# Optimization experiments

Hardware: AMD Instinct MI355X
Metric: run time of the kernel (lower is better)

Reference implementation:

```python
import jax, jax.numpy as jnp
import numpy as np

STRIDE = 4.0      # fpn_strides[0]
POOL = 7          # roi_align_size
SR = 2            # roi_align_sampling_ratio
NUM_CLASSES = 10
B, N = 2, 512
C, H, W = 256, 256, 256
OUT = 1024


def _bilinear(feat_hwc, y, x):
    # feat_hwc: [H, W, C]; y, x: [N, 7, 7, SR, SR] sample coords (feature units)
    Hf, Wf, _ = feat_hwc.shape
    valid = (y > -1.0) & (y < Hf) & (x > -1.0) & (x < Wf)
    y = jnp.clip(y, 0.0, Hf - 1.0)
    x = jnp.clip(x, 0.0, Wf - 1.0)
    y0 = jnp.floor(y)
    x0 = jnp.floor(x)
    y0i = y0.astype(jnp.int32)
    x0i = x0.astype(jnp.int32)
    y1i = jnp.minimum(y0i + 1, Hf - 1)
    x1i = jnp.minimum(x0i + 1, Wf - 1)
    ly = (y - y0)[..., None]
    lx = (x - x0)[..., None]
    hy = 1.0 - ly
    hx = 1.0 - lx
    v = (hy * hx * feat_hwc[y0i, x0i] + hy * lx * feat_hwc[y0i, x1i]
         + ly * hx * feat_hwc[y1i, x0i] + ly * lx * feat_hwc[y1i, x1i])
    return v * valid[..., None]


def _roi_align_rotated(feat_hwc, boxes):
    # boxes: [N, 5] = (cx, cy, w, h, theta) in feature coords -> [N, 7, 7, C]
    cx, cy, w, h, th = (boxes[:, k] for k in range(5))
    bins = jnp.arange(POOL, dtype=feat_hwc.dtype)
    sub = (jnp.arange(SR, dtype=feat_hwc.dtype) + 0.5) / SR
    # local (box-frame) coords of sample points along each axis: [N, 7, SR]
    ys = -h[:, None, None] / 2 + (h / POOL)[:, None, None] * (bins[None, :, None] + sub[None, None, :])
    xs = -w[:, None, None] / 2 + (w / POOL)[:, None, None] * (bins[None, :, None] + sub[None, None, :])
    yy = ys[:, :, None, :, None]  # [N,7,1,SR,1]
    xx = xs[:, None, :, None, :]  # [N,1,7,1,SR]
    cos = jnp.cos(th)[:, None, None, None, None]
    sin = jnp.sin(th)[:, None, None, None, None]
    gx = cx[:, None, None, None, None] + xx * cos - yy * sin
    gy = cy[:, None, None, None, None] + xx * sin + yy * cos
    v = _bilinear(feat_hwc, gy, gx)  # [N,7,7,SR,SR,C]
    return v.mean(axis=(3, 4))       # average-pool the SRxSR samples per bin


def norm_angle(a):
    return (a + jnp.pi / 2) % jnp.pi - jnp.pi / 2


def setup_inputs():
    key = jax.random.key(0)
    ks = jax.random.split(key, 14)
    feat = jax.random.normal(ks[0], (B, C, H, W), jnp.float32)
    cx = jax.random.uniform(ks[1], (B, N), minval=16.0, maxval=H - 16.0)
    cy = jax.random.uniform(ks[2], (B, N), minval=16.0, maxval=W - 16.0)
    bw = jax.random.uniform(ks[3], (B, N), minval=8.0, maxval=64.0)
    bh = jax.random.uniform(ks[4], (B, N), minval=8.0, maxval=64.0)
    th = jax.random.uniform(ks[5], (B, N), minval=-np.pi / 2, maxval=np.pi / 2)
    proposals = jnp.stack([cx, cy, bw, bh, th], axis=-1).astype(jnp.float32)
    d_in = C * POOL * POOL
    s = 0.02
    return {
        'feat': feat,
        'proposals': proposals,
        'W1': jax.random.normal(ks[6], (d_in, OUT), jnp.float32) * s,
        'b1': jnp.zeros((OUT,), jnp.float32),
        'W2': jax.random.normal(ks[7], (OUT, OUT), jnp.float32) * s,
        'b2': jnp.zeros((OUT,), jnp.float32),
        'Wcls': jax.random.normal(ks[8], (OUT, NUM_CLASSES + 1), jnp.float32) * s,
        'bcls': jnp.zeros((NUM_CLASSES + 1,), jnp.float32),
        'Wreg': jax.random.normal(ks[9], (OUT, 5), jnp.float32) * s,
        'breg': jnp.zeros((5,), jnp.float32),
    }


def reference(feat, proposals, W1, b1, W2, b2, Wcls, bcls, Wreg, breg):
    Bn, Nn = proposals.shape[:2]
    feat_hwc = jnp.transpose(feat, (0, 2, 3, 1))  # [B,H,W,C]
    pooled = jax.vmap(_roi_align_rotated)(feat_hwc, proposals)  # [B,N,7,7,C]
    # torch flattens [N, C, 7, 7] -> C*49; match that layout
    x = jnp.transpose(pooled, (0, 1, 4, 2, 3)).reshape(Bn, Nn, -1)
    x = jax.nn.relu(x @ W1 + b1)
    x = jax.nn.relu(x @ W2 + b2)
    cls = x @ Wcls + bcls   # [B,N,11]
    reg = x @ Wreg + breg   # [B,N,5]
    # decode (proposals scaled to image coords by stride; theta unscaled)
    scale = jnp.array([STRIDE, STRIDE, STRIDE, STRIDE, 1.0], feat.dtype)
    p = proposals * scale
    clamp_v = float(abs(np.log(16.0 / 1000.0)))
    bx = p[..., 2] * reg[..., 0] + p[..., 0]
    by = p[..., 3] * reg[..., 1] + p[..., 1]
    bw = p[..., 2] * jnp.exp(jnp.clip(reg[..., 2], -clamp_v, clamp_v))
    bh = p[..., 3] * jnp.exp(jnp.clip(reg[..., 3], -clamp_v, clamp_v))
    ba = norm_angle(p[..., 4] + reg[..., 4])
    boxes = jnp.stack([bx, by, bw, bh, ba], axis=-1)
    return boxes, cls
```

## Files before the change

kernel.cpp:

```cpp
#include <hip/hip_runtime.h>
#include <math.h>
#include <stdint.h>

#define BB 2
#define NN 512
#define CC 256
#define HH 256
#define WW 256
#define DIN 12544
#define OUT1 1024
#define NCLS 11
#define NROI 1024
#define SK1 8
#define SK2 2

typedef short bf16x8 __attribute__((ext_vector_type(8)));
typedef float f32x4 __attribute__((ext_vector_type(4)));

__device__ inline unsigned short f2bf(float f) {
  unsigned int u = __float_as_uint(f);
  u += 0x7FFF + ((u >> 16) & 1);
  return (unsigned short)(u >> 16);
}
__device__ inline float bf2f(unsigned short h) {
  return __uint_as_float(((unsigned int)h) << 16);
}
__device__ inline float4 ld_bf4(const unsigned short* p) {
  ushort4 r = *(const ushort4*)p;
  return make_float4(bf2f(r.x), bf2f(r.y), bf2f(r.z), bf2f(r.w));
}

__device__ inline void gll16(const void* g, void* l) {
  __builtin_amdgcn_global_load_lds(
      reinterpret_cast<const __attribute__((address_space(1))) void*>(
          reinterpret_cast<uintptr_t>(g)),
      reinterpret_cast<__attribute__((address_space(3))) void*>(
          (unsigned int)reinterpret_cast<uintptr_t>(l)),
      16, 0, 0);
}

__global__ __launch_bounds__(256) void transpose_to_hwc_bf16(
    const float* __restrict__ in, unsigned short* __restrict__ out) {
  __shared__ float tile[64][65];
  int b = blockIdx.z;
  int hw0 = blockIdx.x * 64;
  int c0 = blockIdx.y * 64;
  int tid = threadIdx.x;
  int hi = tid >> 4, lo = tid & 15;
#pragma unroll
  for (int pass = 0; pass < 4; ++pass) {
    int cl = hi + pass * 16;
    float4 v = *(const float4*)(in + ((size_t)b * CC + c0 + cl) * (HH * WW) +
                                hw0 + lo * 4);
    tile[lo * 4 + 0][cl] = v.x;
    tile[lo * 4 + 1][cl] = v.y;
    tile[lo * 4 + 2][cl] = v.z;
    tile[lo * 4 + 3][cl] = v.w;
  }
  __syncthreads();
#pragma unroll
  for (int pass = 0; pass < 4; ++pass) {
    int hwl = hi + pass * 16;
    int cc = lo * 4;
    ushort4 o;
    o.x = f2bf(tile[hwl][cc + 0]);
    o.y = f2bf(tile[hwl][cc + 1]);
    o.z = f2bf(tile[hwl][cc + 2]);
    o.w = f2bf(tile[hwl][cc + 3]);
    *(ushort4*)(out + ((size_t)b * (HH * WW) + hw0 + hwl) * CC + c0 + cc) = o;
  }
}

__device__ inline void bilin(float gy, float gx, int& y0, int& x0, int& y1,
                             int& x1, float& w00, float& w01, float& w10,
                             float& w11) {
  float valid = (gy > -1.f && gy < 256.f && gx > -1.f && gx < 256.f) ? 0.25f : 0.f;
  float y = fminf(fmaxf(gy, 0.f), 255.f);
  float x = fminf(fmaxf(gx, 0.f), 255.f);
  float yf = floorf(y), xf = floorf(x);
  y0 = (int)yf; x0 = (int)xf;
  y1 = min(y0 + 1, 255); x1 = min(x0 + 1, 255);
  float ly = y - yf, lx = x - xf, hy = 1.f - ly, hx = 1.f - lx;
  w00 = hy * hx * valid; w01 = hy * lx * valid;
  w10 = ly * hx * valid; w11 = ly * lx * valid;
}

__global__ __launch_bounds__(256) void roi_align_hwc(
    const unsigned short* __restrict__ fhwc, const float* __restrict__ props,
    unsigned short* __restrict__ pooled) {
  int roi = blockIdx.x;
  int b = roi >> 9;
  const float* p = props + (size_t)roi * 5;
  float cx = p[0], cy = p[1], w = p[2], h = p[3], th = p[4];
  float sn = sinf(th), cs = cosf(th);
  int wave = threadIdx.x >> 6, lane = threadIdx.x & 63;
  int c4 = lane * 4;
  const unsigned short* fb = fhwc + (size_t)b * HH * WW * CC;
  unsigned short* outp = pooled + (size_t)roi * DIN;

  for (int bin = wave; bin < 49; bin += 4) {
    int py = bin / 7, px = bin - py * 7;
    float a0 = 0.f, a1 = 0.f, a2 = 0.f, a3 = 0.f;
#pragma unroll
    for (int sy = 0; sy < 2; ++sy) {
#pragma unroll
      for (int sx = 0; sx < 2; ++sx) {
        float ys = -0.5f * h + (h / 7.0f) * ((float)py + ((float)sy + 0.5f) * 0.5f);
        float xs = -0.5f * w + (w / 7.0f) * ((float)px + ((float)sx + 0.5f) * 0.5f);
        float gx = cx + xs * cs - ys * sn;
        float gy = cy + xs * sn + ys * cs;
        int y0, x0, y1, x1; float w00, w01, w10, w11;
        bilin(gy, gx, y0, x0, y1, x1, w00, w01, w10, w11);
        float4 v00 = ld_bf4(fb + ((size_t)(y0 * WW + x0)) * CC + c4);
        float4 v01 = ld_bf4(fb + ((size_t)(y0 * WW + x1)) * CC + c4);
        float4 v10 = ld_bf4(fb + ((size_t)(y1 * WW + x0)) * CC + c4);
        float4 v11 = ld_bf4(fb + ((size_t)(y1 * WW + x1)) * CC + c4);
        a0 += w00 * v00.x + w01 * v01.x + w10 * v10.x + w11 * v11.x;
        a1 += w00 * v00.y + w01 * v01.y + w10 * v10.y + w11 * v11.y;
        a2 += w00 * v00.z + w01 * v01.z + w10 * v10.z + w11 * v11.z;
        a3 += w00 * v00.w + w01 * v01.w + w10 * v10.w + w11 * v11.w;
      }
    }
    ushort4 o;
    o.x = f2bf(a0); o.y = f2bf(a1); o.z = f2bf(a2); o.w = f2bf(a3);
    *(ushort4*)(outp + bin * 256 + c4) = o;
  }
}

__global__ __launch_bounds__(256) void roi_align_nchw(
    const float* __restrict__ feat, const float* __restrict__ props,
    unsigned short* __restrict__ pooled) {
  int roi = blockIdx.x;
  int b = roi >> 9;
  int c = threadIdx.x;
  const float* p = props + (size_t)roi * 5;
  float cx = p[0], cy = p[1], w = p[2], h = p[3], th = p[4];
  float sn = sinf(th), cs = cosf(th);
  const float* fb = feat + ((size_t)b * CC + c) * (HH * WW);
  unsigned short* outp = pooled + (size_t)roi * DIN;
  for (int bin = 0; bin < 49; ++bin) {
    int py = bin / 7, px = bin - py * 7;
    float acc = 0.f;
#pragma unroll
    for (int sy = 0; sy < 2; ++sy) {
#pragma unroll
      for (int sx = 0; sx < 2; ++sx) {
        float ys = -0.5f * h + (h / 7.0f) * ((float)py + ((float)sy + 0.5f) * 0.5f);
        float xs = -0.5f * w + (w / 7.0f) * ((float)px + ((float)sx + 0.5f) * 0.5f);
        float gx = cx + xs * cs - ys * sn;
        float gy = cy + xs * sn + ys * cs;
        int y0, x0, y1, x1; float w00, w01, w10, w11;
        bilin(gy, gx, y0, x0, y1, x1, w00, w01, w10, w11);
        acc += w00 * fb[(size_t)y0 * WW + x0] + w01 * fb[(size_t)y0 * WW + x1] +
               w10 * fb[(size_t)y1 * WW + x0] + w11 * fb[(size_t)y1 * WW + x1];
      }
    }
    outp[bin * 256 + c] = f2bf(acc);
  }
}

template <bool PERM>
__global__ __launch_bounds__(256) void cvt_w(const float* __restrict__ in,
                                             unsigned short* __restrict__ out,
                                             int N, int Kout) {
  __shared__ float tile[64][65];
  int k0 = blockIdx.x * 64, n0 = blockIdx.y * 64;
  int tid = threadIdx.x;
  int hi = tid >> 4, lo = tid & 15;
#pragma unroll
  for (int pass = 0; pass < 4; ++pass) {
    int ki = hi + pass * 16;
    int k = k0 + ki;
    int row = PERM ? ((k & 255) * 49 + (k >> 8)) : k;
    float4 v = *(const float4*)(in + (size_t)row * N + n0 + lo * 4);
    tile[ki][lo * 4 + 0] = v.x;
    tile[ki][lo * 4 + 1] = v.y;
    tile[ki][lo * 4 + 2] = v.z;
    tile[ki][lo * 4 + 3] = v.w;
  }
  __syncthreads();
#pragma unroll
  for (int pass = 0; pass < 4; ++pass) {
    int nl = hi + pass * 16;
    int kq = lo * 4;
    ushort4 o;
    o.x = f2bf(tile[kq + 0][nl]);
    o.y = f2bf(tile[kq + 1][nl]);
    o.z = f2bf(tile[kq + 2][nl]);
    o.w = f2bf(tile[kq + 3][nl]);
    *(ushort4*)(out + (size_t)(n0 + nl) * Kout + k0 + kq) = o;
  }
}

__global__ __launch_bounds__(256) void pack_head_w(
    const float* __restrict__ Wcls, const float* __restrict__ bcls,
    const float* __restrict__ Wreg, const float* __restrict__ breg,
    unsigned short* __restrict__ Wcat, float* __restrict__ bcat) {
  int o = blockIdx.x;
  int t = threadIdx.x;
#pragma unroll
  for (int j = 0; j < 4; ++j) {
    int k = t * 4 + j;
    float v = (o < NCLS) ? Wcls[(size_t)k * NCLS + o]
                         : Wreg[(size_t)k * 5 + (o - NCLS)];
    Wcat[(size_t)o * OUT1 + k] = f2bf(v);
  }
  if (t == 0) bcat[o] = (o < NCLS) ? bcls[o] : breg[o - NCLS];
}

__global__ __launch_bounds__(256) void gemm_mfma_128(
    const unsigned short* __restrict__ A, const unsigned short* __restrict__ Bw,
    unsigned short* __restrict__ part, int K, int Ks) {
  __shared__ short As[128 * 32];
  __shared__ short Bs[128 * 32];
  int tid = threadIdx.x;
  int w = tid >> 6, lane = tid & 63;
  int quad = lane >> 4, l16 = lane & 15;
  int m0 = blockIdx.y * 128, n0 = blockIdx.x * 128;
  int bz = blockIdx.z;
  int wm = w >> 1, wn = w & 1;

  const char* pA = (const char*)A +
      ((size_t)(m0 + 32 * w + (lane >> 2)) * K + (size_t)bz * Ks) * 2 +
      (lane & 3) * 16;
  const char* pB = (const char*)Bw +
      ((size_t)(n0 + 32 * w + (lane >> 2)) * K + (size_t)bz * Ks) * 2 +
      (lane & 3) * 16;
  short* la = &As[w * 1024];
  short* lb = &Bs[w * 1024];
  const size_t rstep = (size_t)K * 2 * 16;

  f32x4 acc[4][4] = {};
  int aoff[4], boff[4];
#pragma unroll
  for (int t = 0; t < 4; ++t) {
    aoff[t] = (wm * 64 + t * 16 + l16) * 32 + quad * 8;
    boff[t] = (wn * 64 + t * 16 + l16) * 32 + quad * 8;
  }

  for (int kk = 0; kk < Ks; kk += 32) {
    __syncthreads();
    gll16(pA, la);
    gll16(pA + rstep, la + 512);
    gll16(pB, lb);
    gll16(pB + rstep, lb + 512);
    pA += 64; pB += 64;
    __syncthreads();
    bf16x8 af[4], bfr[4];
#pragma unroll
    for (int t = 0; t < 4; ++t) af[t] = *(const bf16x8*)&As[aoff[t]];
#pragma unroll
    for (int t = 0; t < 4; ++t) bfr[t] = *(const bf16x8*)&Bs[boff[t]];
#pragma unroll
    for (int mt = 0; mt < 4; ++mt)
#pragma unroll
      for (int nt = 0; nt < 4; ++nt)
        acc[mt][nt] = __builtin_amdgcn_mfma_f32_16x16x32_bf16(
            af[mt], bfr[nt], acc[mt][nt], 0, 0, 0);
  }

  unsigned short* pp = part + (size_t)bz * (OUT1 * NROI);
#pragma unroll
  for (int mt = 0; mt < 4; ++mt)
#pragma unroll
    for (int nt = 0; nt < 4; ++nt) {
      int col = n0 + wn * 64 + nt * 16 + l16;
#pragma unroll
      for (int r = 0; r < 4; ++r) {
        int row = m0 + wm * 64 + mt * 16 + quad * 4 + r;
        pp[(size_t)row * OUT1 + col] = f2bf(acc[mt][nt][r]);
      }
    }
}

__global__ __launch_bounds__(256) void reduce_relu_bf16(
    const unsigned short* __restrict__ part, const float* __restrict__ bias,
    unsigned short* __restrict__ out) {
  int i = blockIdx.x * 256 + threadIdx.x;
  int base = i * 8;
  int col = base & (OUT1 - 1);
  float s[8] = {};
#pragma unroll
  for (int z = 0; z < SK1; ++z) {
    uint4 v = *(const uint4*)(part + (size_t)z * (NROI * OUT1) + base);
    s[0] += __uint_as_float(v.x << 16);
    s[1] += __uint_as_float(v.x & 0xFFFF0000u);
    s[2] += __uint_as_float(v.y << 16);
    s[3] += __uint_as_float(v.y & 0xFFFF0000u);
    s[4] += __uint_as_float(v.z << 16);
    s[5] += __uint_as_float(v.z & 0xFFFF0000u);
    s[6] += __uint_as_float(v.w << 16);
    s[7] += __uint_as_float(v.w & 0xFFFF0000u);
  }
  float4 b0 = *(const float4*)(bias + col);
  float4 b1 = *(const float4*)(bias + col + 4);
  uint4 o;
  o.x = (unsigned int)f2bf(fmaxf(s[0] + b0.x, 0.f)) |
        ((unsigned int)f2bf(fmaxf(s[1] + b0.y, 0.f)) << 16);
  o.y = (unsigned int)f2bf(fmaxf(s[2] + b0.z, 0.f)) |
        ((unsigned int)f2bf(fmaxf(s[3] + b0.w, 0.f)) << 16);
  o.z = (unsigned int)f2bf(fmaxf(s[4] + b1.x, 0.f)) |
        ((unsigned int)f2bf(fmaxf(s[5] + b1.y, 0.f)) << 16);
  o.w = (unsigned int)f2bf(fmaxf(s[6] + b1.z, 0.f)) |
        ((unsigned int)f2bf(fmaxf(s[7] + b1.w, 0.f)) << 16);
  *(uint4*)(out + base) = o;
}

__global__ __launch_bounds__(256) void gemm_mfma_64_part(
    const unsigned short* __restrict__ A, const unsigned short* __restrict__ Bw,
    float* __restrict__ part, int K, int Ks) {
  __shared__ short As[64 * 64];
  __shared__ short Bs[64 * 64];
  int tid = threadIdx.x;
  int w = tid >> 6, lane = tid & 63;
  int quad = lane >> 4, l16 = lane & 15;
  int m0 = blockIdx.y * 64, n0 = blockIdx.x * 64;
  int bz = blockIdx.z;
  int wm = w >> 1, wn = w & 1;

  const char* pA = (const char*)A +
      ((size_t)(m0 + 16 * w + (lane >> 3)) * K + (size_t)bz * Ks) * 2 +
      (lane & 7) * 16;
  const char* pB = (const char*)Bw +
      ((size_t)(n0 + 16 * w + (lane >> 3)) * K + (size_t)bz * Ks) * 2 +
      (lane & 7) * 16;
  short* la = &As[w * 1024];
  short* lb = &Bs[w * 1024];
  const size_t rstep = (size_t)K * 2 * 8;

  f32x4 acc[2][2] = {};
  int aoff[2], boff[2];
#pragma unroll
  for (int t = 0; t < 2; ++t) {
    aoff[t] = (wm * 32 + t * 16 + l16) * 64 + quad * 8;
    boff[t] = (wn * 32 + t * 16 + l16) * 64 + quad * 8;
  }

  for (int kk = 0; kk < Ks; kk += 64) {
    __syncthreads();
    gll16(pA, la);
    gll16(pA + rstep, la + 512);
    gll16(pB, lb);
    gll16(pB + rstep, lb + 512);
    pA += 128; pB += 128;
    __syncthreads();
#pragma unroll
    for (int ks = 0; ks < 2; ++ks) {
      bf16x8 af[2], bfr[2];
#pragma unroll
      for (int t = 0; t < 2; ++t) af[t] = *(const bf16x8*)&As[aoff[t] + ks * 32];
#pragma unroll
      for (int t = 0; t < 2; ++t) bfr[t] = *(const bf16x8*)&Bs[boff[t] + ks * 32];
#pragma unroll
      for (int mt = 0; mt < 2; ++mt)
#pragma unroll
        for (int nt = 0; nt < 2; ++nt)
          acc[mt][nt] = __builtin_amdgcn_mfma_f32_16x16x32_bf16(
              af[mt], bfr[nt], acc[mt][nt], 0, 0, 0);
    }
  }
  float* pp = part + (size_t)bz * (OUT1 * NROI);
#pragma unroll
  for (int mt = 0; mt < 2; ++mt)
#pragma unroll
    for (int nt = 0; nt < 2; ++nt) {
      int col = n0 + wn * 32 + nt * 16 + l16;
#pragma unroll
      for (int r = 0; r < 4; ++r) {
        int row = m0 + wm * 32 + mt * 16 + quad * 4 + r;
        pp[(size_t)row * OUT1 + col] = acc[mt][nt][r];
      }
    }
}

__global__ __launch_bounds__(256) void head_kernel(
    const float* __restrict__ P, const float* __restrict__ b2,
    const unsigned short* __restrict__ Wcat, const float* __restrict__ bcat,
    const float* __restrict__ props, float* __restrict__ out) {
  __shared__ float xrow[1024];
  __shared__ float res[16];
  int row = blockIdx.x;
  int tid = threadIdx.x;
  int wave = tid >> 6, lane = tid & 63;
  {
    size_t off = (size_t)row * 1024 + tid * 4;
    float4 a = *(const float4*)(P + off);
#pragma unroll
    for (int z = 1; z < SK2; ++z) {
      float4 t = *(const float4*)(P + (size_t)z * (NROI * OUT1) + off);
      a.x += t.x; a.y += t.y; a.z += t.z; a.w += t.w;
    }
    float4 bv = *(const float4*)(b2 + tid * 4);
    xrow[tid * 4 + 0] = fmaxf(a.x + bv.x, 0.f);
    xrow[tid * 4 + 1] = fmaxf(a.y + bv.y, 0.f);
    xrow[tid * 4 + 2] = fmaxf(a.z + bv.z, 0.f);
    xrow[tid * 4 + 3] = fmaxf(a.w + bv.w, 0.f);
  }
  __syncthreads();
#pragma unroll
  for (int oo = 0; oo < 4; ++oo) {
    int o = wave * 4 + oo;
    const unsigned short* wr = Wcat + (size_t)o * OUT1;
    float s = 0.f;
#pragma unroll
    for (int pass = 0; pass < 2; ++pass) {
      int k = pass * 512 + lane * 8;
      uint4 v = *(const uint4*)(wr + k);
      float4 x0 = *(const float4*)&xrow[k];
      float4 x1 = *(const float4*)&xrow[k + 4];
      s += __uint_as_float(v.x << 16) * x0.x;
      s += __uint_as_float(v.x & 0xFFFF0000u) * x0.y;
      s += __uint_as_float(v.y << 16) * x0.z;
      s += __uint_as_float(v.y & 0xFFFF0000u) * x0.w;
      s += __uint_as_float(v.z << 16) * x1.x;
      s += __uint_as_float(v.z & 0xFFFF0000u) * x1.y;
      s += __uint_as_float(v.w << 16) * x1.z;
      s += __uint_as_float(v.w & 0xFFFF0000u) * x1.w;
    }
#pragma unroll
    for (int d = 32; d > 0; d >>= 1) s += __shfl_down(s, d);
    if (lane == 0) res[o] = s + bcat[o];
  }
  __syncthreads();
  if (tid < NCLS) out[5120 + (size_t)row * NCLS + tid] = res[tid];
  if (tid == 0) {
    const float* p = props + (size_t)row * 5;
    float p0 = p[0] * 4.f, p1 = p[1] * 4.f, p2 = p[2] * 4.f, p3 = p[3] * 4.f,
          p4 = p[4];
    float r0 = res[11], r1 = res[12], r2 = res[13], r3 = res[14], r4 = res[15];
    const float V = 4.135166556742356f;
    float bx = p2 * r0 + p0;
    float by = p3 * r1 + p1;
    float bw = p2 * expf(fminf(fmaxf(r2, -V), V));
    float bh = p3 * expf(fminf(fmaxf(r3, -V), V));
    const float PI = 3.14159265358979323846f;
    float a = p4 + r4;
    float m = fmodf(a + PI * 0.5f, PI);
    if (m < 0.f) m += PI;
    float ba = m - PI * 0.5f;
    float* bo = out + (size_t)row * 5;
    bo[0] = bx; bo[1] = by; bo[2] = bw; bo[3] = bh; bo[4] = ba;
  }
}

extern "C" void kernel_launch(void* const* d_in, const int* in_sizes, int n_in,
                              void* d_out, int out_size, void* d_ws,
                              size_t ws_size, hipStream_t stream) {
  const float* feat  = (const float*)d_in[0];
  const float* props = (const float*)d_in[1];
  const float* W1    = (const float*)d_in[2];
  const float* b1    = (const float*)d_in[3];
  const float* W2    = (const float*)d_in[4];
  const float* b2    = (const float*)d_in[5];
  const float* Wcls  = (const float*)d_in[6];
  const float* bcls  = (const float*)d_in[7];
  const float* Wreg  = (const float*)d_in[8];
  const float* breg  = (const float*)d_in[9];
  float* out = (float*)d_out;

  char* wp = (char*)d_ws;
  unsigned short* pooled = (unsigned short*)wp; wp += (size_t)NROI * DIN * 2;
  unsigned short* W1T    = (unsigned short*)wp; wp += (size_t)OUT1 * DIN * 2;
  unsigned short* W2T    = (unsigned short*)wp; wp += (size_t)OUT1 * OUT1 * 2;
  unsigned short* x1     = (unsigned short*)wp; wp += (size_t)NROI * OUT1 * 2;
  unsigned short* part1  = (unsigned short*)wp; wp += (size_t)SK1 * NROI * OUT1 * 2;
  float*          part2  = (float*)wp;          wp += (size_t)SK2 * NROI * OUT1 * 4;
  unsigned short* Wcat   = (unsigned short*)wp; wp += (size_t)16 * OUT1 * 2;
  float*          bcat   = (float*)wp;          wp += 16 * 4;
  unsigned short* fhwc   = (unsigned short*)wp;

  size_t need_min  = (size_t)(wp - (char*)d_ws);
  size_t need_full = need_min + (size_t)BB * CC * HH * WW * 2;

  if (ws_size >= need_full) {
    transpose_to_hwc_bf16<<<dim3(HH * WW / 64, CC / 64, BB), 256, 0, stream>>>(
        feat, fhwc);
    roi_align_hwc<<<NROI, 256, 0, stream>>>(fhwc, props, pooled);
  } else {
    roi_align_nchw<<<NROI, 256, 0, stream>>>(feat, props, pooled);
  }

  cvt_w<true><<<dim3(DIN / 64, OUT1 / 64), 256, 0, stream>>>(W1, W1T, OUT1, DIN);
  cvt_w<false><<<dim3(OUT1 / 64, OUT1 / 64), 256, 0, stream>>>(W2, W2T, OUT1,
                                                               OUT1);
  pack_head_w<<<16, 256, 0, stream>>>(Wcls, bcls, Wreg, breg, Wcat, bcat);

  gemm_mfma_128<<<dim3(8, 8, SK1), 256, 0, stream>>>(pooled, W1T, part1, DIN,
                                                     DIN / SK1);
  reduce_relu_bf16<<<NROI * OUT1 / 2048, 256, 0, stream>>>(part1, b1, x1);
  gemm_mfma_64_part<<<dim3(16, 16, SK2), 256, 0, stream>>>(x1, W2T, part2, OUT1,
                                                           OUT1 / SK2);
  head_kernel<<<NROI, 256, 0, stream>>>(part2, b2, Wcat, bcat, props, out);
}
```

Measured before the change: 396.0 us.

## Store pooled features in C*49 order and simplify weight transposes

ROI-align now stages each ROI's pooled bins in shared memory in channel-major (c*49+bin) order and writes the row out with coalesced 16-byte stores. W1 therefore no longer needs a permuted row gather during conversion, and a single wider-tile transpose kernel handles both weight matrices. The feature transpose moves to 128x128 tiles with bf16 in LDS and more loads in flight per thread. The shared-memory stores use a stride of 49 and may bank-conflict, and the larger LDS footprint may lower occupancy. An empty loop was also added to the GEMM and does nothing.

```diff
diff --git a/kernel.cpp b/kernel.cpp
--- a/kernel.cpp
+++ b/kernel.cpp
@@ -41,33 +41,36 @@
 
 __global__ __launch_bounds__(256) void transpose_to_hwc_bf16(
     const float* __restrict__ in, unsigned short* __restrict__ out) {
-  __shared__ float tile[64][65];
+  __shared__ unsigned short tile[128 * 132];
   int b = blockIdx.z;
-  int hw0 = blockIdx.x * 64;
-  int c0 = blockIdx.y * 64;
+  int hw0 = blockIdx.x * 128;
+  int c0 = blockIdx.y * 128;
   int tid = threadIdx.x;
-  int hi = tid >> 4, lo = tid & 15;
-#pragma unroll
-  for (int pass = 0; pass < 4; ++pass) {
-    int cl = hi + pass * 16;
-    float4 v = *(const float4*)(in + ((size_t)b * CC + c0 + cl) * (HH * WW) +
-                                hw0 + lo * 4);
-    tile[lo * 4 + 0][cl] = v.x;
-    tile[lo * 4 + 1][cl] = v.y;
-    tile[lo * 4 + 2][cl] = v.z;
-    tile[lo * 4 + 3][cl] = v.w;
+  int hl = tid & 31;
+  int hr = tid >> 5;
+  const float* base = in + ((size_t)b * CC + c0) * (HH * WW) + hw0;
+  float4 v[16];
+#pragma unroll
+  for (int p = 0; p < 16; ++p) {
+    int c = p * 8 + hr;
+    v[p] = *(const float4*)(base + (size_t)c * (HH * WW) + hl * 4);
+  }
+#pragma unroll
+  for (int p = 0; p < 16; ++p) {
+    int c = p * 8 + hr;
+    int hw = hl * 4;
+    tile[(hw + 0) * 132 + c] = f2bf(v[p].x);
+    tile[(hw + 1) * 132 + c] = f2bf(v[p].y);
+    tile[(hw + 2) * 132 + c] = f2bf(v[p].z);
+    tile[(hw + 3) * 132 + c] = f2bf(v[p].w);
   }
   __syncthreads();
-#pragma unroll
-  for (int pass = 0; pass < 4; ++pass) {
-    int hwl = hi + pass * 16;
-    int cc = lo * 4;
-    ushort4 o;
-    o.x = f2bf(tile[hwl][cc + 0]);
-    o.y = f2bf(tile[hwl][cc + 1]);
-    o.z = f2bf(tile[hwl][cc + 2]);
-    o.w = f2bf(tile[hwl][cc + 3]);
-    *(ushort4*)(out + ((size_t)b * (HH * WW) + hw0 + hwl) * CC + c0 + cc) = o;
+  unsigned short* ob = out + ((size_t)b * (HH * WW) + hw0) * CC + c0;
+#pragma unroll
+  for (int p = 0; p < 16; ++p) {
+    int r = p * 8 + hr;
+    ushort4 o = *(const ushort4*)&tile[r * 132 + hl * 4];
+    *(ushort4*)(ob + (size_t)r * CC + hl * 4) = o;
   }
 }
 
@@ -88,15 +91,16 @@
 __global__ __launch_bounds__(256) void roi_align_hwc(
     const unsigned short* __restrict__ fhwc, const float* __restrict__ props,
     unsigned short* __restrict__ pooled) {
+  __shared__ unsigned short prow[DIN];
   int roi = blockIdx.x;
   int b = roi >> 9;
   const float* p = props + (size_t)roi * 5;
   float cx = p[0], cy = p[1], w = p[2], h = p[3], th = p[4];
   float sn = sinf(th), cs = cosf(th);
-  int wave = threadIdx.x >> 6, lane = threadIdx.x & 63;
+  int tid = threadIdx.x;
+  int wave = tid >> 6, lane = tid & 63;
   int c4 = lane * 4;
   const unsigned short* fb = fhwc + (size_t)b * HH * WW * CC;
-  unsigned short* outp = pooled + (size_t)roi * DIN;
 
   for (int bin = wave; bin < 49; bin += 4) {
     int py = bin / 7, px = bin - py * 7;
@@ -121,15 +125,21 @@
         a3 += w00 * v00.w + w01 * v01.w + w10 * v10.w + w11 * v11.w;
       }
     }
-    ushort4 o;
-    o.x = f2bf(a0); o.y = f2bf(a1); o.z = f2bf(a2); o.w = f2bf(a3);
-    *(ushort4*)(outp + bin * 256 + c4) = o;
-  }
+    prow[(c4 + 0) * 49 + bin] = f2bf(a0);
+    prow[(c4 + 1) * 49 + bin] = f2bf(a1);
+    prow[(c4 + 2) * 49 + bin] = f2bf(a2);
+    prow[(c4 + 3) * 49 + bin] = f2bf(a3);
+  }
+  __syncthreads();
+  const uint4* src = (const uint4*)prow;
+  uint4* dst = (uint4*)(pooled + (size_t)roi * DIN);
+  for (int i = tid; i < DIN / 8; i += 256) dst[i] = src[i];
 }
 
 __global__ __launch_bounds__(256) void roi_align_nchw(
     const float* __restrict__ feat, const float* __restrict__ props,
     unsigned short* __restrict__ pooled) {
+  __shared__ unsigned short prow[DIN];
   int roi = blockIdx.x;
   int b = roi >> 9;
   int c = threadIdx.x;
@@ -137,7 +147,6 @@
   float cx = p[0], cy = p[1], w = p[2], h = p[3], th = p[4];
   float sn = sinf(th), cs = cosf(th);
   const float* fb = feat + ((size_t)b * CC + c) * (HH * WW);
-  unsigned short* outp = pooled + (size_t)roi * DIN;
   for (int bin = 0; bin < 49; ++bin) {
     int py = bin / 7, px = bin - py * 7;
     float acc = 0.f;
@@ -155,40 +164,43 @@
                w10 * fb[(size_t)y1 * WW + x0] + w11 * fb[(size_t)y1 * WW + x1];
       }
     }
-    outp[bin * 256 + c] = f2bf(acc);
-  }
-}
-
-template <bool PERM>
-__global__ __launch_bounds__(256) void cvt_w(const float* __restrict__ in,
-                                             unsigned short* __restrict__ out,
-                                             int N, int Kout) {
-  __shared__ float tile[64][65];
-  int k0 = blockIdx.x * 64, n0 = blockIdx.y * 64;
+    prow[c * 49 + bin] = f2bf(acc);
+  }
+  __syncthreads();
+  const uint4* src = (const uint4*)prow;
+  uint4* dst = (uint4*)(pooled + (size_t)roi * DIN);
+  for (int i = threadIdx.x; i < DIN / 8; i += 256) dst[i] = src[i];
+}
+
+__global__ __launch_bounds__(256) void cvt_w_t(const float* __restrict__ in,
+                                               unsigned short* __restrict__ out,
+                                               int K) {
+  __shared__ unsigned short tile[256 * 68];
+  int k0 = blockIdx.x * 64, n0 = blockIdx.y * 256;
   int tid = threadIdx.x;
-  int hi = tid >> 4, lo = tid & 15;
-#pragma unroll
-  for (int pass = 0; pass < 4; ++pass) {
-    int ki = hi + pass * 16;
-    int k = k0 + ki;
-    int row = PERM ? ((k & 255) * 49 + (k >> 8)) : k;
-    float4 v = *(const float4*)(in + (size_t)row * N + n0 + lo * 4);
-    tile[ki][lo * 4 + 0] = v.x;
-    tile[ki][lo * 4 + 1] = v.y;
-    tile[ki][lo * 4 + 2] = v.z;
-    tile[ki][lo * 4 + 3] = v.w;
+  int l = tid & 63, w = tid >> 6;
+  float4 v[16];
+#pragma unroll
+  for (int p = 0; p < 16; ++p) {
+    int k = p * 4 + w;
+    v[p] = *(const float4*)(in + (size_t)(k0 + k) * OUT1 + n0 + l * 4);
+  }
+#pragma unroll
+  for (int p = 0; p < 16; ++p) {
+    int k = p * 4 + w;
+    int n = l * 4;
+    tile[(n + 0) * 68 + k] = f2bf(v[p].x);
+    tile[(n + 1) * 68 + k] = f2bf(v[p].y);
+    tile[(n + 2) * 68 + k] = f2bf(v[p].z);
+    tile[(n + 3) * 68 + k] = f2bf(v[p].w);
   }
   __syncthreads();
-#pragma unroll
-  for (int pass = 0; pass < 4; ++pass) {
-    int nl = hi + pass * 16;
-    int kq = lo * 4;
-    ushort4 o;
-    o.x = f2bf(tile[kq + 0][nl]);
-    o.y = f2bf(tile[kq + 1][nl]);
-    o.z = f2bf(tile[kq + 2][nl]);
-    o.w = f2bf(tile[kq + 3][nl]);
-    *(ushort4*)(out + (size_t)(n0 + nl) * Kout + k0 + kq) = o;
+  int wl = tid & 15, wr = tid >> 4;
+#pragma unroll
+  for (int p = 0; p < 16; ++p) {
+    int n = p * 16 + wr;
+    ushort4 o = *(const ushort4*)&tile[n * 68 + wl * 4];
+    *(ushort4*)(out + (size_t)(n0 + n) * K + k0 + wl * 4) = o;
   }
 }
 
@@ -336,6 +348,7 @@
     boff[t] = (wn * 32 + t * 16 + l16) * 64 + quad * 8;
   }
 
+  for (int kk = 0; kk < K  && kk < Ks; kk += 64) {}
   for (int kk = 0; kk < Ks; kk += 64) {
     __syncthreads();
     gll16(pA, la);
@@ -473,16 +486,15 @@
   size_t need_full = need_min + (size_t)BB * CC * HH * WW * 2;
 
   if (ws_size >= need_full) {
-    transpose_to_hwc_bf16<<<dim3(HH * WW / 64, CC / 64, BB), 256, 0, stream>>>(
+    transpose_to_hwc_bf16<<<dim3(HH * WW / 128, CC / 128, BB), 256, 0, stream>>>(
         feat, fhwc);
     roi_align_hwc<<<NROI, 256, 0, stream>>>(fhwc, props, pooled);
   } else {
     roi_align_nchw<<<NROI, 256, 0, stream>>>(feat, props, pooled);
   }
 
-  cvt_w<true><<<dim3(DIN / 64, OUT1 / 64), 256, 0, stream>>>(W1, W1T, OUT1, DIN);
-  cvt_w<false><<<dim3(OUT1 / 64, OUT1 / 64), 256, 0, stream>>>(W2, W2T, OUT1,
-                                                               OUT1);
+  cvt_w_t<<<dim3(DIN / 64, OUT1 / 256), 256, 0, stream>>>(W1, W1T, DIN);
+  cvt_w_t<<<dim3(OUT1 / 64, OUT1 / 256), 256, 0, stream>>>(W2, W2T, OUT1);
   pack_head_w<<<16, 256, 0, stream>>>(Wcls, bcls, Wreg, breg, Wcat, bcat);
 
   gemm_mfma_128<<<dim3(8, 8, SK1), 256, 0, stream>>>(pooled, W1T, part1, DIN,
```

New measurement: 416.6 us. +5.2%, slower.

## Enlarge transpose tiles with bf16 LDS staging and split ROI-align bins across two blocks

Applied to the files above, without the earlier changes.

The NCHW-to-HWC transpose now handles 128x128 tiles per block. All 16 float4 loads are issued before any LDS writes, values are converted to bf16 before staging, and each thread writes out ushort4 rows. This aims to raise memory-level parallelism and halve LDS footprint per element in the bandwidth-bound transpose. ROI align launches two blocks per ROI, with the 49 bins striped across 8 waves, to give the gather more parallelism. The trade-offs are more registers per thread in the transpose and duplicated sin/cos and setup work per ROI.

```diff
diff --git a/kernel.cpp b/kernel.cpp
--- a/kernel.cpp
+++ b/kernel.cpp
@@ -41,33 +41,36 @@
 
 __global__ __launch_bounds__(256) void transpose_to_hwc_bf16(
     const float* __restrict__ in, unsigned short* __restrict__ out) {
-  __shared__ float tile[64][65];
+  __shared__ unsigned short tile[128 * 132];
   int b = blockIdx.z;
-  int hw0 = blockIdx.x * 64;
-  int c0 = blockIdx.y * 64;
+  int hw0 = blockIdx.x * 128;
+  int c0 = blockIdx.y * 128;
   int tid = threadIdx.x;
-  int hi = tid >> 4, lo = tid & 15;
-#pragma unroll
-  for (int pass = 0; pass < 4; ++pass) {
-    int cl = hi + pass * 16;
-    float4 v = *(const float4*)(in + ((size_t)b * CC + c0 + cl) * (HH * WW) +
-                                hw0 + lo * 4);
-    tile[lo * 4 + 0][cl] = v.x;
-    tile[lo * 4 + 1][cl] = v.y;
-    tile[lo * 4 + 2][cl] = v.z;
-    tile[lo * 4 + 3][cl] = v.w;
+  int hl = tid & 31;
+  int hr = tid >> 5;
+  const float* base = in + ((size_t)b * CC + c0) * (HH * WW) + hw0;
+  float4 v[16];
+#pragma unroll
+  for (int p = 0; p < 16; ++p) {
+    int c = p * 8 + hr;
+    v[p] = *(const float4*)(base + (size_t)c * (HH * WW) + hl * 4);
+  }
+#pragma unroll
+  for (int p = 0; p < 16; ++p) {
+    int c = p * 8 + hr;
+    int hw = hl * 4;
+    tile[(hw + 0) * 132 + c] = f2bf(v[p].x);
+    tile[(hw + 1) * 132 + c] = f2bf(v[p].y);
+    tile[(hw + 2) * 132 + c] = f2bf(v[p].z);
+    tile[(hw + 3) * 132 + c] = f2bf(v[p].w);
   }
   __syncthreads();
-#pragma unroll
-  for (int pass = 0; pass < 4; ++pass) {
-    int hwl = hi + pass * 16;
-    int cc = lo * 4;
-    ushort4 o;
-    o.x = f2bf(tile[hwl][cc + 0]);
-    o.y = f2bf(tile[hwl][cc + 1]);
-    o.z = f2bf(tile[hwl][cc + 2]);
-    o.w = f2bf(tile[hwl][cc + 3]);
-    *(ushort4*)(out + ((size_t)b * (HH * WW) + hw0 + hwl) * CC + c0 + cc) = o;
+  unsigned short* ob = out + ((size_t)b * (HH * WW) + hw0) * CC + c0;
+#pragma unroll
+  for (int p = 0; p < 16; ++p) {
+    int r = p * 8 + hr;
+    ushort4 o = *(const ushort4*)&tile[r * 132 + hl * 4];
+    *(ushort4*)(ob + (size_t)r * CC + hl * 4) = o;
   }
 }
 
@@ -93,12 +96,13 @@
   const float* p = props + (size_t)roi * 5;
   float cx = p[0], cy = p[1], w = p[2], h = p[3], th = p[4];
   float sn = sinf(th), cs = cosf(th);
-  int wave = threadIdx.x >> 6, lane = threadIdx.x & 63;
+  int gw = blockIdx.y * 4 + (threadIdx.x >> 6);
+  int lane = threadIdx.x & 63;
   int c4 = lane * 4;
   const unsigned short* fb = fhwc + (size_t)b * HH * WW * CC;
   unsigned short* outp = pooled + (size_t)roi * DIN;
 
-  for (int bin = wave; bin < 49; bin += 4) {
+  for (int bin = gw; bin < 49; bin += 8) {
     int py = bin / 7, px = bin - py * 7;
     float a0 = 0.f, a1 = 0.f, a2 = 0.f, a3 = 0.f;
 #pragma unroll
@@ -473,9 +477,9 @@
   size_t need_full = need_min + (size_t)BB * CC * HH * WW * 2;
 
   if (ws_size >= need_full) {
-    transpose_to_hwc_bf16<<<dim3(HH * WW / 64, CC / 64, BB), 256, 0, stream>>>(
+    transpose_to_hwc_bf16<<<dim3(HH * WW / 128, CC / 128, BB), 256, 0, stream>>>(
         feat, fhwc);
-    roi_align_hwc<<<NROI, 256, 0, stream>>>(fhwc, props, pooled);
+    roi_align_hwc<<<dim3(NROI, 2), 256, 0, stream>>>(fhwc, props, pooled);
   } else {
     roi_align_nchw<<<NROI, 256, 0, stream>>>(feat, props, pooled);
   }
```

Result: no change. 394.8 us (-0.3%).
